# Optimization experiments

Measured on AMD Instinct MI355X. Metric: run time of the kernel, lower is better.

Reference implementation:

```python
import jax, jax.numpy as jnp
import numpy as np

N_NODES = 100000
N_EDGES = 1600000
D_IN = 128
D_OUT = 128


def setup_inputs() -> dict:
    key = jax.random.key(0)
    k_x, k_e, k_wl, k_bl, k_wr = jax.random.split(key, 5)
    x = jax.random.normal(k_x, (N_NODES, D_IN), dtype=jnp.float32)
    edge_index = jax.random.randint(k_e, (2, N_EDGES), 0, N_NODES, dtype=jnp.int64)
    # PyG Linear default init ~ kaiming-uniform-ish; plain uniform is fine for a numeric reference
    s = 1.0 / np.sqrt(D_IN)
    W_l = jax.random.uniform(k_wl, (D_OUT, D_IN), minval=-s, maxval=s, dtype=jnp.float32)
    b_l = jax.random.uniform(k_bl, (D_OUT,), minval=-s, maxval=s, dtype=jnp.float32)
    W_r = jax.random.uniform(k_wr, (D_OUT, D_IN), minval=-s, maxval=s, dtype=jnp.float32)
    return {"x": x, "edge_index": edge_index, "W_l": W_l, "b_l": b_l, "W_r": W_r}


def reference(x, edge_index, W_l, b_l, W_r):
    # SAGEConv (mean aggr): messages flow src -> dst
    src = edge_index[0]  # [E]
    dst = edge_index[1]  # [E]
    msgs = x[src]  # [E, D_IN] neighbor gather
    summed = jax.ops.segment_sum(msgs, dst, num_segments=N_NODES)  # [N, D_IN]
    deg = jax.ops.segment_sum(jnp.ones_like(dst, dtype=x.dtype), dst, num_segments=N_NODES)  # [N]
    agg = summed / jnp.maximum(deg, 1.0)[:, None]  # mean with 0 for isolated nodes
    # out = lin_l(agg) + lin_r(x); bias only on lin_l (PyG default)
    out = agg @ W_l.T + b_l + x @ W_r.T
    return out
```

## Files before the change

### kernel.cpp

```cpp
#include <hip/hip_runtime.h>

#define D_FEAT 128
#define CAP 32
#define S1CAP (1 << 16)
#define S2CAP (1 << 16)
#define LOGB 7
#define LOCB 128
#define BCAP 2560
#define CHUNK 4096
#define NBUK_MAX 1024
#define BPAD 8

typedef short bf16x8 __attribute__((ext_vector_type(8)));
typedef float f32x4 __attribute__((ext_vector_type(4)));

__device__ __forceinline__ unsigned short f2bf(float f) {
    unsigned u = __builtin_bit_cast(unsigned, f);
    u += 0x7FFF + ((u >> 16) & 1);
    return (unsigned short)(u >> 16);
}


__global__ __launch_bounds__(256) void tprep_kernel(
    const int* __restrict__ ei, int* __restrict__ flag, int* __restrict__ s1cnt,
    int* __restrict__ s2cnt, int* __restrict__ bincnt) {
    const int b = blockIdx.x;
    const int t = threadIdx.x;
    for (int i = b * 256 + t; i < NBUK_MAX * BPAD; i += 8 * 256) bincnt[i] = 0;
    if (b == 0) {
        __shared__ int nzs[4];
        int nz = 0;
        for (int i = t; i < 4096; i += 256) nz |= (ei[2 * i + 1] != 0);
        unsigned long long bal = __ballot(nz);
        if ((t & 63) == 0) nzs[t >> 6] = (bal != 0ull) ? 1 : 0;
        __syncthreads();
        if (t == 0) {
            *flag = (nzs[0] | nzs[1] | nzs[2] | nzs[3]) ? 0 : 1;
            *s1cnt = 0;
            *s2cnt = 0;
        }
    }
}

__global__ __launch_bounds__(256) void bwx_kernel(
    const int* __restrict__ ei, const int* __restrict__ flag,
    int* __restrict__ bincnt, unsigned* __restrict__ bins,
    int* __restrict__ s1cnt, int* __restrict__ spill1, int E, int N, int NBUK,
    int BINB,
    const float* __restrict__ Wl, const float* __restrict__ Wr,
    unsigned short* __restrict__ Wc,
    const float4* __restrict__ x4, uint2* __restrict__ xb2, long total4) {
    const int b = blockIdx.x;
    const int t = threadIdx.x;

    if (b < BINB) {
        __shared__ int hist[NBUK_MAX];
        __shared__ int rbase[NBUK_MAX];
        __shared__ unsigned ent[CHUNK];
        __shared__ unsigned short ebk[CHUNK];
        const long e0 = (long)b * CHUNK;
        const int cnt = (int)min((long)CHUNK, (long)E - e0);
        const int is64 = *flag;

        for (int i = t; i < NBUK; i += 256) hist[i] = 0;
        __syncthreads();

        for (int i = t; i < cnt; i += 256) {
            long e = e0 + i;
            int src, dst;
            if (is64) {
                src = (int)((const long long*)ei)[e];
                dst = (int)((const long long*)ei)[(long)E + e];
            } else {
                src = ei[e];
                dst = ei[(long)E + e];
            }
            src = min(max(src, 0), N - 1);
            dst = min(max(dst, 0), N - 1);
            int bk = dst >> LOGB;
            ent[i] = ((unsigned)(dst & (LOCB - 1)) << 25) | (unsigned)src;
            ebk[i] = (unsigned short)bk;
            atomicAdd(&hist[bk], 1);
        }
        __syncthreads();

        for (int i = t; i < NBUK; i += 256) {
            int h = hist[i];
            rbase[i] = (h > 0) ? atomicAdd(&bincnt[i * BPAD], h) : 0;
            hist[i] = 0;
        }
        __syncthreads();

        for (int i = t; i < cnt; i += 256) {
            int bk = ebk[i];
            int slot = rbase[bk] + atomicAdd(&hist[bk], 1);
            if (slot < BCAP) {
                bins[(long)bk * BCAP + slot] = ent[i];
            } else {
                unsigned v = ent[i];
                int sp = atomicAdd(s1cnt, 1);
                if (sp < S1CAP) {
                    spill1[2 * sp] = (int)(v & 0x1FFFFFFu);
                    spill1[2 * sp + 1] = (bk << LOGB) | (int)(v >> 25);
                }
            }
        }
    } else if (b < BINB + 128) {
        int n = b - BINB;
        float w = (t < 128) ? Wl[n * 128 + t] : Wr[n * 128 + (t - 128)];
        Wc[n * 256 + t] = f2bf(w);
    } else {
        long gid = (long)(b - BINB - 128) * 256 + t;
        if (gid < total4) {
            float4 v = x4[gid];
            uint2 o;
            o.x = (unsigned)f2bf(v.x) | ((unsigned)f2bf(v.y) << 16);
            o.y = (unsigned)f2bf(v.z) | ((unsigned)f2bf(v.w) << 16);
            xb2[gid] = o;
        }
    }
}

__global__ __launch_bounds__(256) void fill2_kernel(
    const unsigned* __restrict__ bins, const int* __restrict__ bincnt,
    int* __restrict__ adj, int* __restrict__ cursor,
    const int* __restrict__ s1cnt, const int* __restrict__ spill1,
    int* __restrict__ s2cnt, int* __restrict__ spill2, int N) {
    __shared__ int cur[LOCB];
    __shared__ __align__(16) int adjimg[LOCB * CAP];
    const int bk = blockIdx.x;
    const int t = threadIdx.x;
    if (t < LOCB) cur[t] = 0;
    __syncthreads();
    const int cnt = min(bincnt[bk * BPAD], BCAP);
    const int nb = bk << LOGB;
    for (int i = t; i < cnt; i += 256) {
        unsigned v = bins[(long)bk * BCAP + i];
        int src = (int)(v & 0x1FFFFFFu);
        int ld = (int)(v >> 25);
        int slot = atomicAdd(&cur[ld], 1);
        if (slot < CAP) {
            adjimg[ld * CAP + slot] = src;
        } else {
            int sp = atomicAdd(s2cnt, 1);
            if (sp < S2CAP) {
                spill2[2 * sp] = src;
                spill2[2 * sp + 1] = nb + ld;
            }
        }
    }
    const int sc = min(*s1cnt, S1CAP);
    for (int i = t; i < sc; i += 256) {
        int dst = spill1[2 * i + 1];
        if ((dst >> LOGB) == bk) {
            int src = spill1[2 * i];
            int ld = dst & (LOCB - 1);
            int slot = atomicAdd(&cur[ld], 1);
            if (slot < CAP) {
                adjimg[ld * CAP + slot] = src;
            } else {
                int sp = atomicAdd(s2cnt, 1);
                if (sp < S2CAP) {
                    spill2[2 * sp] = src;
                    spill2[2 * sp + 1] = dst;
                }
            }
        }
    }
    __syncthreads();
    const int lim = min(LOCB, N - nb);
    const int nvec = lim * CAP / 4;
    uint4* dstp = (uint4*)&adj[(long)nb * CAP];
    const uint4* srcp = (const uint4*)adjimg;
    for (int i = t; i < nvec; i += 256) dstp[i] = srcp[i];
    if (t < LOCB && nb + t < N) cursor[nb + t] = cur[t];
}

__device__ __forceinline__ void acc_row(float* acc, uint4 v) {
    acc[0] += __builtin_bit_cast(float, v.x << 16);
    acc[1] += __builtin_bit_cast(float, v.x & 0xFFFF0000u);
    acc[2] += __builtin_bit_cast(float, v.y << 16);
    acc[3] += __builtin_bit_cast(float, v.y & 0xFFFF0000u);
    acc[4] += __builtin_bit_cast(float, v.z << 16);
    acc[5] += __builtin_bit_cast(float, v.z & 0xFFFF0000u);
    acc[6] += __builtin_bit_cast(float, v.w << 16);
    acc[7] += __builtin_bit_cast(float, v.w & 0xFFFF0000u);
}

__device__ __forceinline__ int pick_src(int adjv, int adjv2, int e, int cq, int qd) {
    int ec = e & 31;
    int s = __shfl((ec < 16) ? adjv : adjv2, qd * 16 + (ec & 15));
    return (e < cq) ? s : 0;
}

__global__ __launch_bounds__(256) void gg_kernel(
    const unsigned int* __restrict__ xb, const int* __restrict__ cursor,
    const int* __restrict__ adj, const unsigned short* __restrict__ Wc,
    const float* __restrict__ bl, float* __restrict__ out, int N) {
    __shared__ __align__(16) unsigned short A[16 * 264];

    const int t = threadIdx.x;
    const int wv = t >> 6;
    const int lane = t & 63;
    const int n0 = blockIdx.x * 16;
    const int fq = lane & 15;
    const int qd = lane >> 4;

    const int n = n0 + wv * 4 + qd;
    const int nc = min(n, N - 1);

    const int deg = (n < N) ? cursor[n] : 0;
    int adjv = adj[(long)nc * CAP + fq];
    int adjv2 = adj[(long)nc * CAP + 16 + fq];

    unsigned xv[4];
#pragma unroll
    for (int q = 0; q < 4; ++q) {
        int nn = n0 + wv * 4 + q;
        xv[q] = (nn < N) ? xb[(long)nn * 64 + lane] : 0u;
    }

    adjv = min(max(adjv, 0), N - 1);
    adjv2 = min(max(adjv2, 0), N - 1);

    const int cq = min(deg, CAP);
    int mx = max(cq, __shfl_xor(cq, 16));
    mx = max(mx, __shfl_xor(mx, 32));
    mx = (mx + 3) & ~3;

    float acc[8] = {0.f, 0.f, 0.f, 0.f, 0.f, 0.f, 0.f, 0.f};
    uint4 va[4], vb[4];
#pragma unroll
    for (int j = 0; j < 4; ++j) {
        int s = pick_src(adjv, adjv2, j, cq, qd);
        va[j] = *(const uint4*)&xb[(long)s * 64 + fq * 4];
    }
    for (int base = 0; base < mx; base += 4) {
#pragma unroll
        for (int j = 0; j < 4; ++j) {
            int s = pick_src(adjv, adjv2, base + 4 + j, cq, qd);
            vb[j] = *(const uint4*)&xb[(long)s * 64 + fq * 4];
        }
#pragma unroll
        for (int j = 0; j < 4; ++j) {
            if (base + j < cq) acc_row(acc, va[j]);
        }
#pragma unroll
        for (int j = 0; j < 4; ++j) va[j] = vb[j];
    }

    const float iv = 1.0f / (float)max(deg, 1);
    uint4 o;
    o.x = (unsigned)f2bf(acc[0] * iv) | ((unsigned)f2bf(acc[1] * iv) << 16);
    o.y = (unsigned)f2bf(acc[2] * iv) | ((unsigned)f2bf(acc[3] * iv) << 16);
    o.z = (unsigned)f2bf(acc[4] * iv) | ((unsigned)f2bf(acc[5] * iv) << 16);
    o.w = (unsigned)f2bf(acc[6] * iv) | ((unsigned)f2bf(acc[7] * iv) << 16);
    *(uint4*)&A[(wv * 4 + qd) * 264 + fq * 8] = o;
#pragma unroll
    for (int q = 0; q < 4; ++q)
        *(unsigned*)&A[(wv * 4 + q) * 264 + 128 + 2 * lane] = xv[q];
    __syncthreads();

    const int l15 = lane & 15;
    const int quad = lane >> 4;
    f32x4 acc2[2];
    acc2[0] = (f32x4){0.f, 0.f, 0.f, 0.f};
    acc2[1] = (f32x4){0.f, 0.f, 0.f, 0.f};

#pragma unroll
    for (int kc = 0; kc < 8; ++kc) {
        const int k0 = kc * 32;
        bf16x8 af = *(const bf16x8*)&A[l15 * 264 + k0 + quad * 8];
#pragma unroll
        for (int nt = 0; nt < 2; ++nt) {
            int col = wv * 32 + nt * 16 + l15;
            bf16x8 bf = *(const bf16x8*)&Wc[col * 256 + k0 + quad * 8];
            acc2[nt] = __builtin_amdgcn_mfma_f32_16x16x32_bf16(af, bf, acc2[nt], 0, 0, 0);
        }
    }

#pragma unroll
    for (int nt = 0; nt < 2; ++nt) {
        int col = wv * 32 + nt * 16 + l15;
        float bias = bl[col];
#pragma unroll
        for (int r = 0; r < 4; ++r) {
            int node = n0 + quad * 4 + r;
            if (node < N) out[(long)node * 128 + col] = acc2[nt][r] + bias;
        }
    }
}

__global__ __launch_bounds__(256) void spill2_kernel(
    const float* __restrict__ x, const float* __restrict__ Wl,
    const int* __restrict__ cursor, const int* __restrict__ s2cnt,
    const int* __restrict__ spill2, float* __restrict__ out) {
    const int wv = threadIdx.x >> 6;
    const int lane = threadIdx.x & 63;
    const int sc = min(*s2cnt, S2CAP);
    for (int i = blockIdx.x * 4 + wv; i < sc; i += gridDim.x * 4) {
        int src = spill2[2 * i];
        int dst = spill2[2 * i + 1];
        float inv = 1.0f / (float)max(cursor[dst], 1);
#pragma unroll
        for (int cc = 0; cc < 2; ++cc) {
            int c = lane + cc * 64;
            float s = 0.0f;
            for (int k = 0; k < 128; k += 4) {
                float4 w4 = *(const float4*)&Wl[c * 128 + k];
                float4 x4 = *(const float4*)&x[(long)src * 128 + k];
                s += w4.x * x4.x + w4.y * x4.y + w4.z * x4.z + w4.w * x4.w;
            }
            atomicAdd(&out[(long)dst * 128 + c], s * inv);
        }
    }
}

extern "C" void kernel_launch(void* const* d_in, const int* in_sizes, int n_in,
                              void* d_out, int out_size, void* d_ws, size_t ws_size,
                              hipStream_t stream) {
    const float* x = (const float*)d_in[0];
    const int* ei = (const int*)d_in[1];
    const float* Wl = (const float*)d_in[2];
    const float* bl = (const float*)d_in[3];
    const float* Wr = (const float*)d_in[4];
    float* out = (float*)d_out;

    const int N = in_sizes[0] / D_FEAT;
    const int E = in_sizes[1] / 2;
    const int NBUK = (N + LOCB - 1) >> LOGB;
    const int BINB = (E + CHUNK - 1) / CHUNK;

    int* wsI = (int*)d_ws;
    int* flag = wsI;
    int* cursor = flag + 64;
    int* s1cnt = cursor + N;
    int* spill1 = s1cnt + 64;
    int* s2cnt = spill1 + 2 * S1CAP;
    int* spill2 = s2cnt + 64;
    int* bincnt = spill2 + 2 * S2CAP;
    unsigned* bins = (unsigned*)(bincnt + NBUK_MAX * BPAD);
    int* adj = (int*)(bins + (long)NBUK * BCAP);
    unsigned short* Wc = (unsigned short*)(adj + (long)N * CAP);
    unsigned int* xb = (unsigned int*)(Wc + 128 * 256);

    const long total4 = (long)N * 32;
    const int XBB = (int)((total4 + 255) / 256);

    tprep_kernel<<<8, 256, 0, stream>>>(ei, flag, s1cnt, s2cnt, bincnt);
    bwx_kernel<<<BINB + 128 + XBB, 256, 0, stream>>>(
        ei, flag, bincnt, bins, s1cnt, spill1, E, N, NBUK, BINB, Wl, Wr, Wc,
        (const float4*)x, (uint2*)xb, total4);
    fill2_kernel<<<NBUK, 256, 0, stream>>>(bins, bincnt, adj, cursor, s1cnt, spill1,
                                           s2cnt, spill2, N);
    gg_kernel<<<(N + 15) / 16, 256, 0, stream>>>(xb, cursor, adj, Wc, bl, out, N);
    spill2_kernel<<<64, 256, 0, stream>>>(x, Wl, cursor, s2cnt, spill2, out);
}
```

Baseline: 243.9 us.

## Fuse per-bucket adjacency build into gather-GEMM kernel and drop fill/spill2 passes

```diff
diff --git a/kernel.cpp b/kernel.cpp
--- a/kernel.cpp
+++ b/kernel.cpp
@@ -3,11 +3,11 @@
 #define D_FEAT 128
 #define CAP 32
 #define S1CAP (1 << 16)
-#define S2CAP (1 << 16)
 #define LOGB 7
 #define LOCB 128
 #define BCAP 2560
 #define CHUNK 4096
+#define EPT 16
 #define NBUK_MAX 1024
 #define BPAD 8
 
@@ -23,7 +23,7 @@
 
 __global__ __launch_bounds__(256) void tprep_kernel(
     const int* __restrict__ ei, int* __restrict__ flag, int* __restrict__ s1cnt,
-    int* __restrict__ s2cnt, int* __restrict__ bincnt) {
+    int* __restrict__ bincnt) {
     const int b = blockIdx.x;
     const int t = threadIdx.x;
     for (int i = b * 256 + t; i < NBUK_MAX * BPAD; i += 8 * 256) bincnt[i] = 0;
@@ -37,7 +37,6 @@
         if (t == 0) {
             *flag = (nzs[0] | nzs[1] | nzs[2] | nzs[3]) ? 0 : 1;
             *s1cnt = 0;
-            *s2cnt = 0;
         }
     }
 }
@@ -56,8 +55,8 @@
     if (b < BINB) {
         __shared__ int hist[NBUK_MAX];
         __shared__ int rbase[NBUK_MAX];
-        __shared__ unsigned ent[CHUNK];
-        __shared__ unsigned short ebk[CHUNK];
+        unsigned ent[EPT];
+        int ebk[EPT];
         const long e0 = (long)b * CHUNK;
         const int cnt = (int)min((long)CHUNK, (long)E - e0);
         const int is64 = *flag;
@@ -65,22 +64,28 @@
         for (int i = t; i < NBUK; i += 256) hist[i] = 0;
         __syncthreads();
 
-        for (int i = t; i < cnt; i += 256) {
-            long e = e0 + i;
-            int src, dst;
-            if (is64) {
-                src = (int)((const long long*)ei)[e];
-                dst = (int)((const long long*)ei)[(long)E + e];
+#pragma unroll
+        for (int k = 0; k < EPT; ++k) {
+            int i = k * 256 + t;
+            if (i < cnt) {
+                long e = e0 + i;
+                int src, dst;
+                if (is64) {
+                    src = (int)((const long long*)ei)[e];
+                    dst = (int)((const long long*)ei)[(long)E + e];
+                } else {
+                    src = ei[e];
+                    dst = ei[(long)E + e];
+                }
+                src = min(max(src, 0), N - 1);
+                dst = min(max(dst, 0), N - 1);
+                int bk = dst >> LOGB;
+                ent[k] = ((unsigned)(dst & (LOCB - 1)) << 25) | (unsigned)src;
+                ebk[k] = bk;
+                atomicAdd(&hist[bk], 1);
             } else {
-                src = ei[e];
-                dst = ei[(long)E + e];
-            }
-            src = min(max(src, 0), N - 1);
-            dst = min(max(dst, 0), N - 1);
-            int bk = dst >> LOGB;
-            ent[i] = ((unsigned)(dst & (LOCB - 1)) << 25) | (unsigned)src;
-            ebk[i] = (unsigned short)bk;
-            atomicAdd(&hist[bk], 1);
+                ebk[k] = -1;
+            }
         }
         __syncthreads();
 
@@ -91,17 +96,20 @@
         }
         __syncthreads();
 
-        for (int i = t; i < cnt; i += 256) {
-            int bk = ebk[i];
-            int slot = rbase[bk] + atomicAdd(&hist[bk], 1);
-            if (slot < BCAP) {
-                bins[(long)bk * BCAP + slot] = ent[i];
-            } else {
-                unsigned v = ent[i];
-                int sp = atomicAdd(s1cnt, 1);
-                if (sp < S1CAP) {
-                    spill1[2 * sp] = (int)(v & 0x1FFFFFFu);
-                    spill1[2 * sp + 1] = (bk << LOGB) | (int)(v >> 25);
+#pragma unroll
+        for (int k = 0; k < EPT; ++k) {
+            int bk = ebk[k];
+            if (bk >= 0) {
+                int slot = rbase[bk] + atomicAdd(&hist[bk], 1);
+                if (slot < BCAP) {
+                    bins[(long)bk * BCAP + slot] = ent[k];
+                } else {
+                    unsigned v = ent[k];
+                    int sp = atomicAdd(s1cnt, 1);
+                    if (sp < S1CAP) {
+                        spill1[2 * sp] = (int)(v & 0x1FFFFFFu);
+                        spill1[2 * sp + 1] = (bk << LOGB) | (int)(v >> 25);
+                    }
                 }
             }
         }
@@ -121,61 +129,6 @@
     }
 }
 
-__global__ __launch_bounds__(256) void fill2_kernel(
-    const unsigned* __restrict__ bins, const int* __restrict__ bincnt,
-    int* __restrict__ adj, int* __restrict__ cursor,
-    const int* __restrict__ s1cnt, const int* __restrict__ spill1,
-    int* __restrict__ s2cnt, int* __restrict__ spill2, int N) {
-    __shared__ int cur[LOCB];
-    __shared__ __align__(16) int adjimg[LOCB * CAP];
-    const int bk = blockIdx.x;
-    const int t = threadIdx.x;
-    if (t < LOCB) cur[t] = 0;
-    __syncthreads();
-    const int cnt = min(bincnt[bk * BPAD], BCAP);
-    const int nb = bk << LOGB;
-    for (int i = t; i < cnt; i += 256) {
-        unsigned v = bins[(long)bk * BCAP + i];
-        int src = (int)(v & 0x1FFFFFFu);
-        int ld = (int)(v >> 25);
-        int slot = atomicAdd(&cur[ld], 1);
-        if (slot < CAP) {
-            adjimg[ld * CAP + slot] = src;
-        } else {
-            int sp = atomicAdd(s2cnt, 1);
-            if (sp < S2CAP) {
-                spill2[2 * sp] = src;
-                spill2[2 * sp + 1] = nb + ld;
-            }
-        }
-    }
-    const int sc = min(*s1cnt, S1CAP);
-    for (int i = t; i < sc; i += 256) {
-        int dst = spill1[2 * i + 1];
-        if ((dst >> LOGB) == bk) {
-            int src = spill1[2 * i];
-            int ld = dst & (LOCB - 1);
-            int slot = atomicAdd(&cur[ld], 1);
-            if (slot < CAP) {
-                adjimg[ld * CAP + slot] = src;
-            } else {
-                int sp = atomicAdd(s2cnt, 1);
-                if (sp < S2CAP) {
-                    spill2[2 * sp] = src;
-                    spill2[2 * sp + 1] = dst;
-                }
-            }
-        }
-    }
-    __syncthreads();
-    const int lim = min(LOCB, N - nb);
-    const int nvec = lim * CAP / 4;
-    uint4* dstp = (uint4*)&adj[(long)nb * CAP];
-    const uint4* srcp = (const uint4*)adjimg;
-    for (int i = t; i < nvec; i += 256) dstp[i] = srcp[i];
-    if (t < LOCB && nb + t < N) cursor[nb + t] = cur[t];
-}
-
 __device__ __forceinline__ void acc_row(float* acc, uint4 v) {
     acc[0] += __builtin_bit_cast(float, v.x << 16);
     acc[1] += __builtin_bit_cast(float, v.x & 0xFFFF0000u);
@@ -187,31 +140,47 @@
     acc[7] += __builtin_bit_cast(float, v.w & 0xFFFF0000u);
 }
 
-__device__ __forceinline__ int pick_src(int adjv, int adjv2, int e, int cq, int qd) {
-    int ec = e & 31;
-    int s = __shfl((ec < 16) ? adjv : adjv2, qd * 16 + (ec & 15));
-    return (e < cq) ? s : 0;
-}
-
 __global__ __launch_bounds__(256) void gg_kernel(
-    const unsigned int* __restrict__ xb, const int* __restrict__ cursor,
-    const int* __restrict__ adj, const unsigned short* __restrict__ Wc,
-    const float* __restrict__ bl, float* __restrict__ out, int N) {
+    const unsigned int* __restrict__ xb, const unsigned* __restrict__ bins,
+    const int* __restrict__ bincnt, const int* __restrict__ s1cnt,
+    const int* __restrict__ spill1, const unsigned short* __restrict__ Wc,
+    const float* __restrict__ bl, float* __restrict__ out, int N, int STRIDE,
+    int NBUK) {
     __shared__ __align__(16) unsigned short A[16 * 264];
-
+    __shared__ int cnt16[16];
+    __shared__ int adjimg[16 * CAP];
+
+    const int g = blockIdx.x % STRIDE;
+    const int j = blockIdx.x / STRIDE;
+    if (g >= NBUK) return;
     const int t = threadIdx.x;
     const int wv = t >> 6;
     const int lane = t & 63;
-    const int n0 = blockIdx.x * 16;
     const int fq = lane & 15;
     const int qd = lane >> 4;
-
-    const int n = n0 + wv * 4 + qd;
-    const int nc = min(n, N - 1);
-
-    const int deg = (n < N) ? cursor[n] : 0;
-    int adjv = adj[(long)nc * CAP + fq];
-    int adjv2 = adj[(long)nc * CAP + 16 + fq];
+    const int n0 = g * LOCB + j * 16;
+    const int ldb = j * 16;
+
+    if (t < 16) cnt16[t] = 0;
+    __syncthreads();
+
+    const int cntE = min(bincnt[g * BPAD], BCAP);
+    for (int i = t; i < cntE; i += 256) {
+        unsigned v = bins[(long)g * BCAP + i];
+        unsigned d = (v >> 25) - (unsigned)ldb;
+        if (d < 16u) {
+            int slot = atomicAdd(&cnt16[d], 1);
+            if (slot < CAP) adjimg[d * CAP + slot] = (int)(v & 0x1FFFFFFu);
+        }
+    }
+    const int sc = min(*s1cnt, S1CAP);
+    for (int i = t; i < sc; i += 256) {
+        unsigned d = (unsigned)(spill1[2 * i + 1] - n0);
+        if (d < 16u) {
+            int slot = atomicAdd(&cnt16[d], 1);
+            if (slot < CAP) adjimg[d * CAP + slot] = spill1[2 * i];
+        }
+    }
 
     unsigned xv[4];
 #pragma unroll
@@ -219,34 +188,52 @@
         int nn = n0 + wv * 4 + q;
         xv[q] = (nn < N) ? xb[(long)nn * 64 + lane] : 0u;
     }
-
-    adjv = min(max(adjv, 0), N - 1);
-    adjv2 = min(max(adjv2, 0), N - 1);
-
-    const int cq = min(deg, CAP);
-    int mx = max(cq, __shfl_xor(cq, 16));
-    mx = max(mx, __shfl_xor(mx, 32));
-    mx = (mx + 3) & ~3;
-
+    __syncthreads();
+
+    const int r = wv * 4 + qd;
+    const int n = n0 + r;
+    const int deg = cnt16[r];
     float acc[8] = {0.f, 0.f, 0.f, 0.f, 0.f, 0.f, 0.f, 0.f};
-    uint4 va[4], vb[4];
-#pragma unroll
-    for (int j = 0; j < 4; ++j) {
-        int s = pick_src(adjv, adjv2, j, cq, qd);
-        va[j] = *(const uint4*)&xb[(long)s * 64 + fq * 4];
-    }
-    for (int base = 0; base < mx; base += 4) {
-#pragma unroll
-        for (int j = 0; j < 4; ++j) {
-            int s = pick_src(adjv, adjv2, base + 4 + j, cq, qd);
-            vb[j] = *(const uint4*)&xb[(long)s * 64 + fq * 4];
-        }
-#pragma unroll
-        for (int j = 0; j < 4; ++j) {
-            if (base + j < cq) acc_row(acc, va[j]);
-        }
-#pragma unroll
-        for (int j = 0; j < 4; ++j) va[j] = vb[j];
+
+    if (deg > 0 && n < N) {
+        if (deg <= CAP) {
+            const int cq = deg;
+            const int mx = (cq + 3) & ~3;
+            uint4 va[4], vb[4];
+#pragma unroll
+            for (int k = 0; k < 4; ++k) {
+                int s = adjimg[r * CAP + min(k, cq - 1)];
+                va[k] = *(const uint4*)&xb[(long)s * 64 + fq * 4];
+            }
+            for (int base = 0; base < mx; base += 4) {
+#pragma unroll
+                for (int k = 0; k < 4; ++k) {
+                    int s = adjimg[r * CAP + min(base + 4 + k, cq - 1)];
+                    vb[k] = *(const uint4*)&xb[(long)s * 64 + fq * 4];
+                }
+#pragma unroll
+                for (int k = 0; k < 4; ++k) {
+                    if (base + k < cq) acc_row(acc, va[k]);
+                }
+#pragma unroll
+                for (int k = 0; k < 4; ++k) va[k] = vb[k];
+            }
+        } else {
+            const int myld = ldb + r;
+            for (int e = 0; e < cntE; ++e) {
+                unsigned v = bins[(long)g * BCAP + e];
+                if ((int)(v >> 25) == myld) {
+                    int s = (int)(v & 0x1FFFFFFu);
+                    acc_row(acc, *(const uint4*)&xb[(long)s * 64 + fq * 4]);
+                }
+            }
+            for (int i = 0; i < sc; ++i) {
+                if (spill1[2 * i + 1] == n) {
+                    int s = spill1[2 * i];
+                    acc_row(acc, *(const uint4*)&xb[(long)s * 64 + fq * 4]);
+                }
+            }
+        }
     }
 
     const float iv = 1.0f / (float)max(deg, 1);
@@ -255,7 +242,7 @@
     o.y = (unsigned)f2bf(acc[2] * iv) | ((unsigned)f2bf(acc[3] * iv) << 16);
     o.z = (unsigned)f2bf(acc[4] * iv) | ((unsigned)f2bf(acc[5] * iv) << 16);
     o.w = (unsigned)f2bf(acc[6] * iv) | ((unsigned)f2bf(acc[7] * iv) << 16);
-    *(uint4*)&A[(wv * 4 + qd) * 264 + fq * 8] = o;
+    *(uint4*)&A[r * 264 + fq * 8] = o;
 #pragma unroll
     for (int q = 0; q < 4; ++q)
         *(unsigned*)&A[(wv * 4 + q) * 264 + 128 + 2 * lane] = xv[q];
@@ -284,34 +271,9 @@
         int col = wv * 32 + nt * 16 + l15;
         float bias = bl[col];
 #pragma unroll
-        for (int r = 0; r < 4; ++r) {
-            int node = n0 + quad * 4 + r;
-            if (node < N) out[(long)node * 128 + col] = acc2[nt][r] + bias;
-        }
-    }
-}
-
-__global__ __launch_bounds__(256) void spill2_kernel(
-    const float* __restrict__ x, const float* __restrict__ Wl,
-    const int* __restrict__ cursor, const int* __restrict__ s2cnt,
-    const int* __restrict__ spill2, float* __restrict__ out) {
-    const int wv = threadIdx.x >> 6;
-    const int lane = threadIdx.x & 63;
-    const int sc = min(*s2cnt, S2CAP);
-    for (int i = blockIdx.x * 4 + wv; i < sc; i += gridDim.x * 4) {
-        int src = spill2[2 * i];
-        int dst = spill2[2 * i + 1];
-        float inv = 1.0f / (float)max(cursor[dst], 1);
-#pragma unroll
-        for (int cc = 0; cc < 2; ++cc) {
-            int c = lane + cc * 64;
-            float s = 0.0f;
-            for (int k = 0; k < 128; k += 4) {
-                float4 w4 = *(const float4*)&Wl[c * 128 + k];
-                float4 x4 = *(const float4*)&x[(long)src * 128 + k];
-                s += w4.x * x4.x + w4.y * x4.y + w4.z * x4.z + w4.w * x4.w;
-            }
-            atomicAdd(&out[(long)dst * 128 + c], s * inv);
+        for (int rr = 0; rr < 4; ++rr) {
+            int node = n0 + quad * 4 + rr;
+            if (node < N) out[(long)node * 128 + col] = acc2[nt][rr] + bias;
         }
     }
 }
@@ -330,29 +292,24 @@
     const int E = in_sizes[1] / 2;
     const int NBUK = (N + LOCB - 1) >> LOGB;
     const int BINB = (E + CHUNK - 1) / CHUNK;
+    const int STRIDE = (NBUK + 7) & ~7;
 
     int* wsI = (int*)d_ws;
     int* flag = wsI;
-    int* cursor = flag + 64;
-    int* s1cnt = cursor + N;
+    int* s1cnt = flag + 64;
     int* spill1 = s1cnt + 64;
-    int* s2cnt = spill1 + 2 * S1CAP;
-    int* spill2 = s2cnt + 64;
-    int* bincnt = spill2 + 2 * S2CAP;
+    int* bincnt = spill1 + 2 * S1CAP;
     unsigned* bins = (unsigned*)(bincnt + NBUK_MAX * BPAD);
-    int* adj = (int*)(bins + (long)NBUK * BCAP);
-    unsigned short* Wc = (unsigned short*)(adj + (long)N * CAP);
+    unsigned short* Wc = (unsigned short*)(bins + (long)NBUK * BCAP);
     unsigned int* xb = (unsigned int*)(Wc + 128 * 256);
 
     const long total4 = (long)N * 32;
     const int XBB = (int)((total4 + 255) / 256);
 
-    tprep_kernel<<<8, 256, 0, stream>>>(ei, flag, s1cnt, s2cnt, bincnt);
+    tprep_kernel<<<8, 256, 0, stream>>>(ei, flag, s1cnt, bincnt);
     bwx_kernel<<<BINB + 128 + XBB, 256, 0, stream>>>(
         ei, flag, bincnt, bins, s1cnt, spill1, E, N, NBUK, BINB, Wl, Wr, Wc,
         (const float4*)x, (uint2*)xb, total4);
-    fill2_kernel<<<NBUK, 256, 0, stream>>>(bins, bincnt, adj, cursor, s1cnt, spill1,
-                                           s2cnt, spill2, N);
-    gg_kernel<<<(N + 15) / 16, 256, 0, stream>>>(xb, cursor, adj, Wc, bl, out, N);
-    spill2_kernel<<<64, 256, 0, stream>>>(x, Wl, cursor, s2cnt, spill2, out);
-}
+    gg_kernel<<<8 * STRIDE, 256, 0, stream>>>(xb, bins, bincnt, s1cnt, spill1, Wc,
+                                              bl, out, N, STRIDE, NBUK);
+}
```

New measurement: 349.3 us. 43.2% more time.

## Replace global atomic bucket binning with per-chunk local sort and offset table

Applied to the files above, without the earlier changes.

```diff
diff --git a/kernel.cpp b/kernel.cpp
--- a/kernel.cpp
+++ b/kernel.cpp
@@ -2,14 +2,13 @@
 
 #define D_FEAT 128
 #define CAP 32
-#define S1CAP (1 << 16)
 #define S2CAP (1 << 16)
 #define LOGB 7
 #define LOCB 128
-#define BCAP 2560
 #define CHUNK 4096
+#define EPT 16
 #define NBUK_MAX 1024
-#define BPAD 8
+#define OSTR 1032
 
 typedef short bf16x8 __attribute__((ext_vector_type(8)));
 typedef float f32x4 __attribute__((ext_vector_type(4)));
@@ -22,89 +21,102 @@
 
 
 __global__ __launch_bounds__(256) void tprep_kernel(
-    const int* __restrict__ ei, int* __restrict__ flag, int* __restrict__ s1cnt,
-    int* __restrict__ s2cnt, int* __restrict__ bincnt) {
-    const int b = blockIdx.x;
+    const int* __restrict__ ei, int* __restrict__ flag, int* __restrict__ s2cnt) {
     const int t = threadIdx.x;
-    for (int i = b * 256 + t; i < NBUK_MAX * BPAD; i += 8 * 256) bincnt[i] = 0;
-    if (b == 0) {
-        __shared__ int nzs[4];
-        int nz = 0;
-        for (int i = t; i < 4096; i += 256) nz |= (ei[2 * i + 1] != 0);
-        unsigned long long bal = __ballot(nz);
-        if ((t & 63) == 0) nzs[t >> 6] = (bal != 0ull) ? 1 : 0;
-        __syncthreads();
-        if (t == 0) {
-            *flag = (nzs[0] | nzs[1] | nzs[2] | nzs[3]) ? 0 : 1;
-            *s1cnt = 0;
-            *s2cnt = 0;
-        }
+    __shared__ int nzs[4];
+    int nz = 0;
+    for (int i = t; i < 4096; i += 256) nz |= (ei[2 * i + 1] != 0);
+    unsigned long long bal = __ballot(nz);
+    if ((t & 63) == 0) nzs[t >> 6] = (bal != 0ull) ? 1 : 0;
+    __syncthreads();
+    if (t == 0) {
+        *flag = (nzs[0] | nzs[1] | nzs[2] | nzs[3]) ? 0 : 1;
+        *s2cnt = 0;
     }
 }
 
 __global__ __launch_bounds__(256) void bwx_kernel(
     const int* __restrict__ ei, const int* __restrict__ flag,
-    int* __restrict__ bincnt, unsigned* __restrict__ bins,
-    int* __restrict__ s1cnt, int* __restrict__ spill1, int E, int N, int NBUK,
-    int BINB,
+    unsigned short* __restrict__ offs2, unsigned* __restrict__ bins2,
+    int E, int N, int NBUK, int BINB,
     const float* __restrict__ Wl, const float* __restrict__ Wr,
     unsigned short* __restrict__ Wc,
     const float4* __restrict__ x4, uint2* __restrict__ xb2, long total4) {
+    __shared__ int hist[NBUK_MAX + 8];
+    __shared__ int wsum[256];
+    __shared__ unsigned sorted[CHUNK];
     const int b = blockIdx.x;
     const int t = threadIdx.x;
 
     if (b < BINB) {
-        __shared__ int hist[NBUK_MAX];
-        __shared__ int rbase[NBUK_MAX];
-        __shared__ unsigned ent[CHUNK];
-        __shared__ unsigned short ebk[CHUNK];
         const long e0 = (long)b * CHUNK;
         const int cnt = (int)min((long)CHUNK, (long)E - e0);
         const int is64 = *flag;
 
-        for (int i = t; i < NBUK; i += 256) hist[i] = 0;
-        __syncthreads();
-
-        for (int i = t; i < cnt; i += 256) {
-            long e = e0 + i;
-            int src, dst;
-            if (is64) {
-                src = (int)((const long long*)ei)[e];
-                dst = (int)((const long long*)ei)[(long)E + e];
+        for (int i = t; i < NBUK_MAX + 8; i += 256) hist[i] = 0;
+        __syncthreads();
+
+        unsigned ent[EPT];
+        int ebk[EPT];
+#pragma unroll
+        for (int k = 0; k < EPT; ++k) {
+            int i = k * 256 + t;
+            if (i < cnt) {
+                long e = e0 + i;
+                int src, dst;
+                if (is64) {
+                    src = (int)((const long long*)ei)[e];
+                    dst = (int)((const long long*)ei)[(long)E + e];
+                } else {
+                    src = ei[e];
+                    dst = ei[(long)E + e];
+                }
+                src = min(max(src, 0), N - 1);
+                dst = min(max(dst, 0), N - 1);
+                int bk = dst >> LOGB;
+                ent[k] = ((unsigned)(dst & (LOCB - 1)) << 25) | (unsigned)src;
+                ebk[k] = bk;
+                atomicAdd(&hist[bk], 1);
             } else {
-                src = ei[e];
-                dst = ei[(long)E + e];
+                ebk[k] = -1;
             }
-            src = min(max(src, 0), N - 1);
-            dst = min(max(dst, 0), N - 1);
-            int bk = dst >> LOGB;
-            ent[i] = ((unsigned)(dst & (LOCB - 1)) << 25) | (unsigned)src;
-            ebk[i] = (unsigned short)bk;
-            atomicAdd(&hist[bk], 1);
-        }
-        __syncthreads();
-
-        for (int i = t; i < NBUK; i += 256) {
-            int h = hist[i];
-            rbase[i] = (h > 0) ? atomicAdd(&bincnt[i * BPAD], h) : 0;
-            hist[i] = 0;
-        }
-        __syncthreads();
-
-        for (int i = t; i < cnt; i += 256) {
-            int bk = ebk[i];
-            int slot = rbase[bk] + atomicAdd(&hist[bk], 1);
-            if (slot < BCAP) {
-                bins[(long)bk * BCAP + slot] = ent[i];
-            } else {
-                unsigned v = ent[i];
-                int sp = atomicAdd(s1cnt, 1);
-                if (sp < S1CAP) {
-                    spill1[2 * sp] = (int)(v & 0x1FFFFFFu);
-                    spill1[2 * sp + 1] = (bk << LOGB) | (int)(v >> 25);
-                }
+        }
+        __syncthreads();
+
+        int v0 = hist[4 * t], v1 = hist[4 * t + 1], v2 = hist[4 * t + 2],
+            v3 = hist[4 * t + 3];
+        int s = v0 + v1 + v2 + v3;
+        wsum[t] = s;
+        __syncthreads();
+        for (int off = 1; off < 256; off <<= 1) {
+            int a = (t >= off) ? wsum[t - off] : 0;
+            __syncthreads();
+            wsum[t] += a;
+            __syncthreads();
+        }
+        int base = wsum[t] - s;
+        hist[4 * t] = base;
+        hist[4 * t + 1] = base + v0;
+        hist[4 * t + 2] = base + v0 + v1;
+        hist[4 * t + 3] = base + v0 + v1 + v2;
+        __syncthreads();
+        unsigned short* orow = offs2 + (long)b * OSTR;
+        for (int i = t; i <= NBUK; i += 256) orow[i] = (unsigned short)hist[i];
+        __syncthreads();
+
+#pragma unroll
+        for (int k = 0; k < EPT; ++k) {
+            if (ebk[k] >= 0) {
+                int slot = atomicAdd(&hist[ebk[k]], 1);
+                sorted[slot] = ent[k];
             }
         }
+        __syncthreads();
+
+        uint4* dstp = (uint4*)(bins2 + (long)b * CHUNK);
+        const uint4* srcp = (const uint4*)sorted;
+#pragma unroll
+        for (int k = 0; k < CHUNK / 4 / 256; ++k) dstp[k * 256 + t] = srcp[k * 256 + t];
     } else if (b < BINB + 128) {
         int n = b - BINB;
         float w = (t < 128) ? Wl[n * 128 + t] : Wr[n * 128 + (t - 128)];
@@ -122,47 +134,32 @@
 }
 
 __global__ __launch_bounds__(256) void fill2_kernel(
-    const unsigned* __restrict__ bins, const int* __restrict__ bincnt,
+    const unsigned* __restrict__ bins2, const unsigned short* __restrict__ offs2,
     int* __restrict__ adj, int* __restrict__ cursor,
-    const int* __restrict__ s1cnt, const int* __restrict__ spill1,
-    int* __restrict__ s2cnt, int* __restrict__ spill2, int N) {
+    int* __restrict__ s2cnt, int* __restrict__ spill2, int N, int NCHUNK) {
     __shared__ int cur[LOCB];
     __shared__ __align__(16) int adjimg[LOCB * CAP];
     const int bk = blockIdx.x;
     const int t = threadIdx.x;
     if (t < LOCB) cur[t] = 0;
     __syncthreads();
-    const int cnt = min(bincnt[bk * BPAD], BCAP);
     const int nb = bk << LOGB;
-    for (int i = t; i < cnt; i += 256) {
-        unsigned v = bins[(long)bk * BCAP + i];
-        int src = (int)(v & 0x1FFFFFFu);
-        int ld = (int)(v >> 25);
-        int slot = atomicAdd(&cur[ld], 1);
-        if (slot < CAP) {
-            adjimg[ld * CAP + slot] = src;
-        } else {
-            int sp = atomicAdd(s2cnt, 1);
-            if (sp < S2CAP) {
-                spill2[2 * sp] = src;
-                spill2[2 * sp + 1] = nb + ld;
-            }
-        }
-    }
-    const int sc = min(*s1cnt, S1CAP);
-    for (int i = t; i < sc; i += 256) {
-        int dst = spill1[2 * i + 1];
-        if ((dst >> LOGB) == bk) {
-            int src = spill1[2 * i];
-            int ld = dst & (LOCB - 1);
+    for (int b = t; b < NCHUNK; b += 256) {
+        const unsigned short* orow = offs2 + (long)b * OSTR;
+        int o0 = orow[bk];
+        int o1 = orow[bk + 1];
+        const unsigned* reg = bins2 + (long)b * CHUNK;
+        for (int k = o0; k < o1; ++k) {
+            unsigned v = reg[k];
+            int ld = (int)(v >> 25);
             int slot = atomicAdd(&cur[ld], 1);
             if (slot < CAP) {
-                adjimg[ld * CAP + slot] = src;
+                adjimg[ld * CAP + slot] = (int)(v & 0x1FFFFFFu);
             } else {
                 int sp = atomicAdd(s2cnt, 1);
                 if (sp < S2CAP) {
-                    spill2[2 * sp] = src;
-                    spill2[2 * sp + 1] = dst;
+                    spill2[2 * sp] = (int)(v & 0x1FFFFFFu);
+                    spill2[2 * sp + 1] = nb + ld;
                 }
             }
         }
@@ -329,30 +326,28 @@
     const int N = in_sizes[0] / D_FEAT;
     const int E = in_sizes[1] / 2;
     const int NBUK = (N + LOCB - 1) >> LOGB;
-    const int BINB = (E + CHUNK - 1) / CHUNK;
+    const int NCHUNK = (E + CHUNK - 1) / CHUNK;
 
     int* wsI = (int*)d_ws;
     int* flag = wsI;
-    int* cursor = flag + 64;
-    int* s1cnt = cursor + N;
-    int* spill1 = s1cnt + 64;
-    int* s2cnt = spill1 + 2 * S1CAP;
+    int* s2cnt = flag + 64;
     int* spill2 = s2cnt + 64;
-    int* bincnt = spill2 + 2 * S2CAP;
-    unsigned* bins = (unsigned*)(bincnt + NBUK_MAX * BPAD);
-    int* adj = (int*)(bins + (long)NBUK * BCAP);
+    int* cursor = spill2 + 2 * S2CAP;
+    unsigned short* offs2 = (unsigned short*)(cursor + N);
+    unsigned* bins2 = (unsigned*)(offs2 + (long)NCHUNK * OSTR + 64);
+    int* adj = (int*)(bins2 + (long)NCHUNK * CHUNK);
     unsigned short* Wc = (unsigned short*)(adj + (long)N * CAP);
     unsigned int* xb = (unsigned int*)(Wc + 128 * 256);
 
     const long total4 = (long)N * 32;
     const int XBB = (int)((total4 + 255) / 256);
 
-    tprep_kernel<<<8, 256, 0, stream>>>(ei, flag, s1cnt, s2cnt, bincnt);
-    bwx_kernel<<<BINB + 128 + XBB, 256, 0, stream>>>(
-        ei, flag, bincnt, bins, s1cnt, spill1, E, N, NBUK, BINB, Wl, Wr, Wc,
+    tprep_kernel<<<1, 256, 0, stream>>>(ei, flag, s2cnt);
+    bwx_kernel<<<NCHUNK + 128 + XBB, 256, 0, stream>>>(
+        ei, flag, offs2, bins2, E, N, NBUK, NCHUNK, Wl, Wr, Wc,
         (const float4*)x, (uint2*)xb, total4);
-    fill2_kernel<<<NBUK, 256, 0, stream>>>(bins, bincnt, adj, cursor, s1cnt, spill1,
-                                           s2cnt, spill2, N);
+    fill2_kernel<<<NBUK, 256, 0, stream>>>(bins2, offs2, adj, cursor, s2cnt, spill2,
+                                           N, NCHUNK);
     gg_kernel<<<(N + 15) / 16, 256, 0, stream>>>(xb, cursor, adj, Wc, bl, out, N);
     spill2_kernel<<<64, 256, 0, stream>>>(x, Wl, cursor, s2cnt, spill2, out);
 }
```

Measured after the change: 248.8 us. +2.0%, slower.
